# Kernel optimization log

Measured on AMD Instinct MI355X. Metric: run time of the kernel, lower is better.

## Reference

```python
import jax, jax.numpy as jnp
import numpy as np

N_NODES = 100000
N_EDGES = 3200000
N_FEAT = 256
N_HID = 64


def setup_inputs() -> dict:
    key = jax.random.key(0)
    k1, k2, k3, k4, k5 = jax.random.split(key, 5)
    edge_index = jax.random.randint(k1, (2, N_EDGES), 0, N_NODES, dtype=jnp.int64 if jax.config.jax_enable_x64 else jnp.int32)
    x = jax.random.normal(k2, (N_NODES, N_FEAT), dtype=jnp.float32)
    s_est = 1.0 / np.sqrt(N_FEAT)
    W_est = jax.random.uniform(k3, (N_FEAT, 1), jnp.float32, -s_est, s_est)
    b_est = jnp.zeros((1,), jnp.float32)
    W_gnn = jax.random.uniform(k4, (N_FEAT, N_HID), jnp.float32, -s_est, s_est)
    b_gnn = jnp.zeros((N_HID,), jnp.float32)
    s_cls = 1.0 / np.sqrt(N_HID)
    W_cls = jax.random.uniform(k5, (N_HID, 1), jnp.float32, -s_cls, s_cls)
    b_cls = jnp.zeros((1,), jnp.float32)
    return {"edge_index": edge_index, "x": x, "W_est": W_est, "b_est": b_est,
            "W_gnn": W_gnn, "b_gnn": b_gnn, "W_cls": W_cls, "b_cls": b_cls}


def _gcn_norm(edge_index, n):
    # PyG GCNConv default: add self-loops, symmetric normalization D^-1/2 (A+I) D^-1/2
    loops = jnp.arange(n, dtype=edge_index.dtype)
    row = jnp.concatenate([edge_index[0], loops])  # source
    col = jnp.concatenate([edge_index[1], loops])  # target
    deg = jax.ops.segment_sum(jnp.ones_like(col, dtype=jnp.float32), col, num_segments=n)
    dinv = jnp.where(deg > 0, jax.lax.rsqrt(jnp.maximum(deg, 1.0)), 0.0)
    norm = dinv[row] * dinv[col]  # [E+N]
    return row, col, norm


def _gcn_conv(x, W, b, row, col, norm, n):
    h = x @ W                              # [N, out] transform first (PyG order)
    msg = norm[:, None] * h[row]           # gather over sources, [E+N, out]
    out = jax.ops.segment_sum(msg, col, num_segments=n)  # scatter-add to targets
    return out + b


def reference(edge_index, x, W_est, b_est, W_gnn, b_gnn, W_cls, b_cls):
    n = x.shape[0]
    row, col, norm = _gcn_norm(edge_index, n)
    s = _gcn_conv(x, W_est, b_est, row, col, norm, n)   # estimator: GCNConv(nfeat, 1)
    z = _gcn_conv(x, W_gnn, b_gnn, row, col, norm, n)   # GNN: GCNConv(nfeat, 64)
    y = z @ W_cls + b_cls                                # classifier head
    return (y, s)
```

## Files before the change

kernel.cpp:

```cpp
#include <hip/hip_runtime.h>

#define N_NODES 100000
#define N_EDGES 3200000
#define N_FEAT  256
#define N_HID   64

#define NBINS     256
#define BIN_W     391
#define BIN_CAP   13568
#define NPART     1000
#define EPB       3200
#define I4PB      800
#define NPQ       25000
#define CPT       4

__global__ void k_wcomb(const float* __restrict__ Wg, const float* __restrict__ bg,
                        const float* __restrict__ Wc, const float* __restrict__ bc,
                        float* __restrict__ wcomb, float* __restrict__ biasy) {
    int f = threadIdx.x;
    float s = 0.f;
#pragma unroll
    for (int k = 0; k < N_HID; ++k) s += Wg[f * N_HID + k] * Wc[k];
    wcomb[f] = s;
    if (f == 0) {
        float b = 0.f;
        for (int k = 0; k < N_HID; ++k) b += bg[k] * Wc[k];
        *biasy = b + bc[0];
    }
}

__global__ __launch_bounds__(256) void k_pqhist(
        const float* __restrict__ x, const float* __restrict__ West,
        const float* __restrict__ wcomb, float2* __restrict__ pq,
        const int4* __restrict__ col4, int* __restrict__ hist) {
    __shared__ int h[NBINS];
    int tid = threadIdx.x;

    if (blockIdx.x >= NPART) {
        int node = (((int)blockIdx.x - NPART) << 2) + (tid >> 6);
        int lane = tid & 63;
        if (node >= N_NODES) return;
        float4 v  = ((const float4*)(x + (size_t)node * N_FEAT))[lane];
        float4 we = ((const float4*)West)[lane];
        float4 wc = ((const float4*)wcomb)[lane];
        float ps = v.x * we.x + v.y * we.y + v.z * we.z + v.w * we.w;
        float qs = v.x * wc.x + v.y * wc.y + v.z * wc.z + v.w * wc.w;
#pragma unroll
        for (int off = 32; off > 0; off >>= 1) {
            ps += __shfl_down(ps, off);
            qs += __shfl_down(qs, off);
        }
        if (lane == 0) pq[node] = make_float2(qs, ps);
        return;
    }

    h[tid] = 0;
    __syncthreads();
    int i0 = blockIdx.x * I4PB;
    for (int i = i0 + tid; i < i0 + I4PB; i += 256) {
        int4 c = col4[i];
        atomicAdd(&h[c.x / BIN_W], 1);
        atomicAdd(&h[c.y / BIN_W], 1);
        atomicAdd(&h[c.z / BIN_W], 1);
        atomicAdd(&h[c.w / BIN_W], 1);
    }
    __syncthreads();
    hist[blockIdx.x * NBINS + tid] = h[tid];
}

__global__ __launch_bounds__(256) void k_scan(const int* __restrict__ hist,
                                              int* __restrict__ base,
                                              int* __restrict__ cursor) {
    __shared__ int ps[256];
    int b = blockIdx.x, t = threadIdx.x;
    int v[CPT];
    int sum = 0;
    int c0 = t * CPT;
#pragma unroll
    for (int j = 0; j < CPT; ++j) {
        int blk = c0 + j;
        v[j] = (blk < NPART) ? hist[blk * NBINS + b] : 0;
        sum += v[j];
    }
    ps[t] = sum;
    __syncthreads();
#pragma unroll
    for (int d = 1; d < 256; d <<= 1) {
        int x = (t >= d) ? ps[t - d] : 0;
        __syncthreads();
        ps[t] += x;
        __syncthreads();
    }
    int run = ps[t] - sum;
#pragma unroll
    for (int j = 0; j < CPT; ++j) {
        int blk = c0 + j;
        if (blk < NPART) { base[blk * NBINS + b] = run; run += v[j]; }
    }
    if (t == 255) cursor[b] = ps[255];
}

__global__ __launch_bounds__(256) void k_scatter(const int4* __restrict__ row4,
                                                 const int4* __restrict__ col4,
                                                 const int* __restrict__ hist,
                                                 const int* __restrict__ base,
                                                 unsigned int* __restrict__ grouped) {
    __shared__ int cnts[NBINS];
    __shared__ int lstart[NBINS];
    __shared__ int lcount[NBINS];
    __shared__ int gbase[NBINS];
    __shared__ int scan[NBINS];
    __shared__ unsigned int stage[EPB];
    int tid = threadIdx.x;
    int cnt = hist[blockIdx.x * NBINS + tid];
    cnts[tid]   = cnt;
    gbase[tid]  = base[blockIdx.x * NBINS + tid];
    scan[tid]   = cnt;
    lcount[tid] = 0;
    __syncthreads();
#pragma unroll
    for (int d = 1; d < 256; d <<= 1) {
        int t = (tid >= d) ? scan[tid - d] : 0;
        __syncthreads();
        scan[tid] += t;
        __syncthreads();
    }
    lstart[tid] = scan[tid] - cnt;
    __syncthreads();

    int i0 = blockIdx.x * I4PB;
    for (int i = i0 + tid; i < i0 + I4PB; i += 256) {
        int4 c = col4[i];
        int4 r = row4[i];
        int b0 = c.x / BIN_W; int s0 = lstart[b0] + atomicAdd(&lcount[b0], 1);
        stage[s0] = ((unsigned)(c.x - b0 * BIN_W) << 17) | (unsigned)r.x;
        int b1 = c.y / BIN_W; int s1 = lstart[b1] + atomicAdd(&lcount[b1], 1);
        stage[s1] = ((unsigned)(c.y - b1 * BIN_W) << 17) | (unsigned)r.y;
        int b2 = c.z / BIN_W; int s2 = lstart[b2] + atomicAdd(&lcount[b2], 1);
        stage[s2] = ((unsigned)(c.z - b2 * BIN_W) << 17) | (unsigned)r.z;
        int b3 = c.w / BIN_W; int s3 = lstart[b3] + atomicAdd(&lcount[b3], 1);
        stage[s3] = ((unsigned)(c.w - b3 * BIN_W) << 17) | (unsigned)r.w;
    }
    __syncthreads();

    int wid = tid >> 6, lane = tid & 63;
    for (int b = wid; b < NBINS; b += 4) {
        int s = lstart[b], len = cnts[b], gb = gbase[b];
        unsigned int* dst = grouped + (size_t)b * BIN_CAP + gb;
        for (int off = lane; off < len; off += 64)
            if (gb + off < BIN_CAP) dst[off] = stage[s + off];
    }
}

__global__ __launch_bounds__(256) void k_bindeg(const int* __restrict__ cursor,
                                                const unsigned int* __restrict__ grouped,
                                                const float2* __restrict__ pq,
                                                float* __restrict__ dinv,
                                                float2* __restrict__ table) {
    __shared__ int dh[BIN_W];
    int b = blockIdx.x, tid = threadIdx.x;
    for (int i = tid; i < BIN_W; i += 256) dh[i] = 0;
    __syncthreads();
    int cnt = cursor[b];
    if (cnt > BIN_CAP) cnt = BIN_CAP;
    const unsigned int* g = grouped + (size_t)b * BIN_CAP;
    for (int i = tid; i < cnt; i += 256) atomicAdd(&dh[g[i] >> 17], 1);
    __syncthreads();
    for (int l = tid; l < BIN_W; l += 256) {
        int node = b * BIN_W + l;
        if (node < N_NODES) {
            float di = rsqrtf((float)(dh[l] + 1));
            dinv[node] = di;
            float2 v = pq[node];
            table[node] = make_float2(di * v.x, di * v.y);
        }
    }
}

__global__ __launch_bounds__(1024) void k_binacc(const int* __restrict__ cursor,
                                                 const unsigned int* __restrict__ grouped,
                                                 const float2* __restrict__ table,
                                                 const float* __restrict__ dinv,
                                                 const float* __restrict__ biasy,
                                                 const float* __restrict__ best,
                                                 float* __restrict__ out) {
    __shared__ float tx[BIN_W];
    __shared__ float ty[BIN_W];
    int b = blockIdx.x, tid = threadIdx.x;
    for (int l = tid; l < BIN_W; l += 1024) {
        int node = b * BIN_W + l;
        float2 t = (node < N_NODES) ? table[node] : make_float2(0.f, 0.f);
        tx[l] = t.x;
        ty[l] = t.y;
    }
    __syncthreads();
    int cnt = cursor[b];
    if (cnt > BIN_CAP) cnt = BIN_CAP;
    const unsigned int* g = grouped + (size_t)b * BIN_CAP;
    const uint2* g2 = (const uint2*)g;
    int n2 = cnt >> 1;
    for (int i = tid; i < n2; i += 1024) {
        uint2 v = g2[i];
        float2 ta = table[v.x & 0x1FFFFu];
        float2 tb = table[v.y & 0x1FFFFu];
        int la = v.x >> 17, lb = v.y >> 17;
        atomicAdd(&tx[la], ta.x);
        atomicAdd(&ty[la], ta.y);
        atomicAdd(&tx[lb], tb.x);
        atomicAdd(&ty[lb], tb.y);
    }
    if (tid == 0 && (cnt & 1)) {
        unsigned int v = g[cnt - 1];
        float2 t = table[v & 0x1FFFFu];
        atomicAdd(&tx[v >> 17], t.x);
        atomicAdd(&ty[v >> 17], t.y);
    }
    __syncthreads();
    float by = biasy[0], bs = best[0];
    for (int l = tid; l < BIN_W; l += 1024) {
        int node = b * BIN_W + l;
        if (node < N_NODES) {
            float di = dinv[node];
            out[node]           = di * tx[l] + by;
            out[N_NODES + node] = di * ty[l] + bs;
        }
    }
}

__global__ __launch_bounds__(256) void k_deg_fb(const int* __restrict__ col,
                                                int* __restrict__ deg) {
    int e = blockIdx.x * blockDim.x + threadIdx.x;
    if (e < N_EDGES) atomicAdd(&deg[col[e]], 1);
}
__global__ __launch_bounds__(256) void k_pqtable_fb(
        const float* __restrict__ x, const float* __restrict__ West,
        const float* __restrict__ wcomb, const int* __restrict__ deg,
        float* __restrict__ dinv, float2* __restrict__ table,
        float2* __restrict__ acc) {
    int node = (blockIdx.x * blockDim.x + threadIdx.x) >> 6;
    int lane = threadIdx.x & 63;
    if (node >= N_NODES) return;
    float4 v  = ((const float4*)(x + (size_t)node * N_FEAT))[lane];
    float4 we = ((const float4*)West)[lane];
    float4 wc = ((const float4*)wcomb)[lane];
    float ps = v.x * we.x + v.y * we.y + v.z * we.z + v.w * we.w;
    float qs = v.x * wc.x + v.y * wc.y + v.z * wc.z + v.w * wc.w;
#pragma unroll
    for (int off = 32; off > 0; off >>= 1) {
        ps += __shfl_down(ps, off);
        qs += __shfl_down(qs, off);
    }
    if (lane == 0) {
        float di = rsqrtf((float)(deg[node] + 1));
        float2 t = make_float2(di * qs, di * ps);
        dinv[node] = di; table[node] = t; acc[node] = t;
    }
}
__global__ __launch_bounds__(256) void k_edge_fb(const int* __restrict__ ei,
                                                 const float2* __restrict__ table,
                                                 float2* __restrict__ acc) {
    int e = blockIdx.x * blockDim.x + threadIdx.x;
    if (e >= N_EDGES) return;
    float2 t = table[ei[e]];
    int c = ei[N_EDGES + e];
    unsafeAtomicAdd(&acc[c].x, t.x);
    unsafeAtomicAdd(&acc[c].y, t.y);
}
__global__ __launch_bounds__(256) void k_fin_fb(
        const float* __restrict__ dinv, const float2* __restrict__ acc,
        const float* __restrict__ biasy, const float* __restrict__ best,
        float* __restrict__ out) {
    int i = blockIdx.x * blockDim.x + threadIdx.x;
    if (i >= N_NODES) return;
    float di = dinv[i];
    float2 a = acc[i];
    out[i]           = di * a.x + biasy[0];
    out[N_NODES + i] = di * a.y + best[0];
}

extern "C" void kernel_launch(void* const* d_in, const int* in_sizes, int n_in,
                              void* d_out, int out_size, void* d_ws, size_t ws_size,
                              hipStream_t stream) {
    const int*   ei   = (const int*)d_in[0];
    const float* x    = (const float*)d_in[1];
    const float* West = (const float*)d_in[2];
    const float* best = (const float*)d_in[3];
    const float* Wg   = (const float*)d_in[4];
    const float* bg   = (const float*)d_in[5];
    const float* Wc   = (const float*)d_in[6];
    const float* bc   = (const float*)d_in[7];
    float* out = (float*)d_out;

    char* ws = (char*)d_ws;
    float*  wcomb = (float*)ws;
    float*  biasy = wcomb + 256;
    float2* pq    = (float2*)(ws + 2048);
    float2* table = (float2*)(ws + 802048);
    float*  dinv  = (float*)(ws + 1602048);
    int*    cursor= (int*)(ws + 2002048);
    unsigned int* grouped = (unsigned int*)(ws + 2003072);
    int*    hist  = (int*)(ws + 2003072 + (size_t)NBINS * BIN_CAP * 4);
    int*    base  = hist + (size_t)NPART * NBINS;
    size_t need = 2003072 + (size_t)NBINS * BIN_CAP * 4 + (size_t)NPART * NBINS * 8;

    if (ws_size >= need) {
        k_wcomb<<<1, 256, 0, stream>>>(Wg, bg, Wc, bc, wcomb, biasy);
        k_pqhist<<<NPART + NPQ, 256, 0, stream>>>(x, West, wcomb, pq,
                                                  (const int4*)(ei + N_EDGES), hist);
        k_scan<<<NBINS, 256, 0, stream>>>(hist, base, cursor);
        k_scatter<<<NPART, 256, 0, stream>>>((const int4*)ei,
                                             (const int4*)(ei + N_EDGES),
                                             hist, base, grouped);
        k_bindeg<<<NBINS, 256, 0, stream>>>(cursor, grouped, pq, dinv, table);
        k_binacc<<<NBINS, 1024, 0, stream>>>(cursor, grouped, table, dinv,
                                             biasy, best, out);
    } else {
        int*    deg  = (int*)(ws + 2048 + 800000 * 2 + 400000);
        float2* acc  = pq;
        float2* tbl  = table;
        hipMemsetAsync(deg, 0, N_NODES * sizeof(int), stream);
        k_wcomb<<<1, 256, 0, stream>>>(Wg, bg, Wc, bc, wcomb, biasy);
        k_deg_fb<<<(N_EDGES + 255) / 256, 256, 0, stream>>>(ei + N_EDGES, deg);
        k_pqtable_fb<<<(N_NODES * 64 + 255) / 256, 256, 0, stream>>>(
            x, West, wcomb, deg, dinv, tbl, acc);
        k_edge_fb<<<(N_EDGES + 255) / 256, 256, 0, stream>>>(ei, tbl, acc);
        k_fin_fb<<<(N_NODES + 255) / 256, 256, 0, stream>>>(dinv, acc, biasy, best, out);
    }
}
```

Measured before the change: 107.7 us.

## Fuse weight combine into histogram kernel and move node matvec into scatter

The tiny weight-combination kernel is folded into block 0 of the histogram kernel, removing one launch. The per-node x·w projection blocks move from the histogram kernel to the scatter kernel, so the histogram and scan run shorter and the dense read of x overlaps with the edge scatter. The projection blocks now inherit the scatter kernel's larger shared-memory footprint, which may reduce occupancy for the bandwidth-bound x read.

```diff
diff --git a/kernel.cpp b/kernel.cpp
--- a/kernel.cpp
+++ b/kernel.cpp
@@ -14,26 +14,82 @@
 #define NPQ       25000
 #define CPT       4
 
-__global__ void k_wcomb(const float* __restrict__ Wg, const float* __restrict__ bg,
-                        const float* __restrict__ Wc, const float* __restrict__ bc,
-                        float* __restrict__ wcomb, float* __restrict__ biasy) {
-    int f = threadIdx.x;
-    float s = 0.f;
-#pragma unroll
-    for (int k = 0; k < N_HID; ++k) s += Wg[f * N_HID + k] * Wc[k];
-    wcomb[f] = s;
-    if (f == 0) {
-        float b = 0.f;
-        for (int k = 0; k < N_HID; ++k) b += bg[k] * Wc[k];
-        *biasy = b + bc[0];
-    }
-}
-
-__global__ __launch_bounds__(256) void k_pqhist(
+__global__ __launch_bounds__(256) void k_histw(
+        const int4* __restrict__ col4, int* __restrict__ hist,
+        const float* __restrict__ Wg, const float* __restrict__ bg,
+        const float* __restrict__ Wc, const float* __restrict__ bc,
+        float* __restrict__ wcomb, float* __restrict__ biasy) {
+    __shared__ int h[NBINS];
+    int tid = threadIdx.x;
+    if (blockIdx.x == 0) {
+        float s = 0.f;
+#pragma unroll
+        for (int k = 0; k < N_HID; ++k) s += Wg[tid * N_HID + k] * Wc[k];
+        wcomb[tid] = s;
+        if (tid == 0) {
+            float b = 0.f;
+            for (int k = 0; k < N_HID; ++k) b += bg[k] * Wc[k];
+            *biasy = b + bc[0];
+        }
+    }
+    h[tid] = 0;
+    __syncthreads();
+    int i0 = blockIdx.x * I4PB;
+    for (int i = i0 + tid; i < i0 + I4PB; i += 256) {
+        int4 c = col4[i];
+        atomicAdd(&h[c.x / BIN_W], 1);
+        atomicAdd(&h[c.y / BIN_W], 1);
+        atomicAdd(&h[c.z / BIN_W], 1);
+        atomicAdd(&h[c.w / BIN_W], 1);
+    }
+    __syncthreads();
+    hist[blockIdx.x * NBINS + tid] = h[tid];
+}
+
+__global__ __launch_bounds__(256) void k_scan(const int* __restrict__ hist,
+                                              int* __restrict__ base,
+                                              int* __restrict__ cursor) {
+    __shared__ int ps[256];
+    int b = blockIdx.x, t = threadIdx.x;
+    int v[CPT];
+    int sum = 0;
+    int c0 = t * CPT;
+#pragma unroll
+    for (int j = 0; j < CPT; ++j) {
+        int blk = c0 + j;
+        v[j] = (blk < NPART) ? hist[blk * NBINS + b] : 0;
+        sum += v[j];
+    }
+    ps[t] = sum;
+    __syncthreads();
+#pragma unroll
+    for (int d = 1; d < 256; d <<= 1) {
+        int x = (t >= d) ? ps[t - d] : 0;
+        __syncthreads();
+        ps[t] += x;
+        __syncthreads();
+    }
+    int run = ps[t] - sum;
+#pragma unroll
+    for (int j = 0; j < CPT; ++j) {
+        int blk = c0 + j;
+        if (blk < NPART) { base[blk * NBINS + b] = run; run += v[j]; }
+    }
+    if (t == 255) cursor[b] = ps[255];
+}
+
+__global__ __launch_bounds__(256) void k_scatpq(
+        const int4* __restrict__ row4, const int4* __restrict__ col4,
+        const int* __restrict__ hist, const int* __restrict__ base,
+        unsigned int* __restrict__ grouped,
         const float* __restrict__ x, const float* __restrict__ West,
-        const float* __restrict__ wcomb, float2* __restrict__ pq,
-        const int4* __restrict__ col4, int* __restrict__ hist) {
-    __shared__ int h[NBINS];
+        const float* __restrict__ wcomb, float2* __restrict__ pq) {
+    __shared__ int cnts[NBINS];
+    __shared__ int lstart[NBINS];
+    __shared__ int lcount[NBINS];
+    __shared__ int gbase[NBINS];
+    __shared__ int scan[NBINS];
+    __shared__ unsigned int stage[EPB];
     int tid = threadIdx.x;
 
     if (blockIdx.x >= NPART) {
@@ -54,64 +110,6 @@
         return;
     }
 
-    h[tid] = 0;
-    __syncthreads();
-    int i0 = blockIdx.x * I4PB;
-    for (int i = i0 + tid; i < i0 + I4PB; i += 256) {
-        int4 c = col4[i];
-        atomicAdd(&h[c.x / BIN_W], 1);
-        atomicAdd(&h[c.y / BIN_W], 1);
-        atomicAdd(&h[c.z / BIN_W], 1);
-        atomicAdd(&h[c.w / BIN_W], 1);
-    }
-    __syncthreads();
-    hist[blockIdx.x * NBINS + tid] = h[tid];
-}
-
-__global__ __launch_bounds__(256) void k_scan(const int* __restrict__ hist,
-                                              int* __restrict__ base,
-                                              int* __restrict__ cursor) {
-    __shared__ int ps[256];
-    int b = blockIdx.x, t = threadIdx.x;
-    int v[CPT];
-    int sum = 0;
-    int c0 = t * CPT;
-#pragma unroll
-    for (int j = 0; j < CPT; ++j) {
-        int blk = c0 + j;
-        v[j] = (blk < NPART) ? hist[blk * NBINS + b] : 0;
-        sum += v[j];
-    }
-    ps[t] = sum;
-    __syncthreads();
-#pragma unroll
-    for (int d = 1; d < 256; d <<= 1) {
-        int x = (t >= d) ? ps[t - d] : 0;
-        __syncthreads();
-        ps[t] += x;
-        __syncthreads();
-    }
-    int run = ps[t] - sum;
-#pragma unroll
-    for (int j = 0; j < CPT; ++j) {
-        int blk = c0 + j;
-        if (blk < NPART) { base[blk * NBINS + b] = run; run += v[j]; }
-    }
-    if (t == 255) cursor[b] = ps[255];
-}
-
-__global__ __launch_bounds__(256) void k_scatter(const int4* __restrict__ row4,
-                                                 const int4* __restrict__ col4,
-                                                 const int* __restrict__ hist,
-                                                 const int* __restrict__ base,
-                                                 unsigned int* __restrict__ grouped) {
-    __shared__ int cnts[NBINS];
-    __shared__ int lstart[NBINS];
-    __shared__ int lcount[NBINS];
-    __shared__ int gbase[NBINS];
-    __shared__ int scan[NBINS];
-    __shared__ unsigned int stage[EPB];
-    int tid = threadIdx.x;
     int cnt = hist[blockIdx.x * NBINS + tid];
     cnts[tid]   = cnt;
     gbase[tid]  = base[blockIdx.x * NBINS + tid];
@@ -227,6 +225,20 @@
     }
 }
 
+__global__ void k_wcomb_fb(const float* __restrict__ Wg, const float* __restrict__ bg,
+                           const float* __restrict__ Wc, const float* __restrict__ bc,
+                           float* __restrict__ wcomb, float* __restrict__ biasy) {
+    int f = threadIdx.x;
+    float s = 0.f;
+#pragma unroll
+    for (int k = 0; k < N_HID; ++k) s += Wg[f * N_HID + k] * Wc[k];
+    wcomb[f] = s;
+    if (f == 0) {
+        float b = 0.f;
+        for (int k = 0; k < N_HID; ++k) b += bg[k] * Wc[k];
+        *biasy = b + bc[0];
+    }
+}
 __global__ __launch_bounds__(256) void k_deg_fb(const int* __restrict__ col,
                                                 int* __restrict__ deg) {
     int e = blockIdx.x * blockDim.x + threadIdx.x;
@@ -304,13 +316,13 @@
     size_t need = 2003072 + (size_t)NBINS * BIN_CAP * 4 + (size_t)NPART * NBINS * 8;
 
     if (ws_size >= need) {
-        k_wcomb<<<1, 256, 0, stream>>>(Wg, bg, Wc, bc, wcomb, biasy);
-        k_pqhist<<<NPART + NPQ, 256, 0, stream>>>(x, West, wcomb, pq,
-                                                  (const int4*)(ei + N_EDGES), hist);
+        k_histw<<<NPART, 256, 0, stream>>>((const int4*)(ei + N_EDGES), hist,
+                                           Wg, bg, Wc, bc, wcomb, biasy);
         k_scan<<<NBINS, 256, 0, stream>>>(hist, base, cursor);
-        k_scatter<<<NPART, 256, 0, stream>>>((const int4*)ei,
-                                             (const int4*)(ei + N_EDGES),
-                                             hist, base, grouped);
+        k_scatpq<<<NPART + NPQ, 256, 0, stream>>>((const int4*)ei,
+                                                  (const int4*)(ei + N_EDGES),
+                                                  hist, base, grouped,
+                                                  x, West, wcomb, pq);
         k_bindeg<<<NBINS, 256, 0, stream>>>(cursor, grouped, pq, dinv, table);
         k_binacc<<<NBINS, 1024, 0, stream>>>(cursor, grouped, table, dinv,
                                              biasy, best, out);
@@ -319,7 +331,7 @@
         float2* acc  = pq;
         float2* tbl  = table;
         hipMemsetAsync(deg, 0, N_NODES * sizeof(int), stream);
-        k_wcomb<<<1, 256, 0, stream>>>(Wg, bg, Wc, bc, wcomb, biasy);
+        k_wcomb_fb<<<1, 256, 0, stream>>>(Wg, bg, Wc, bc, wcomb, biasy);
         k_deg_fb<<<(N_EDGES + 255) / 256, 256, 0, stream>>>(ei + N_EDGES, deg);
         k_pqtable_fb<<<(N_NODES * 64 + 255) / 256, 256, 0, stream>>>(
             x, West, wcomb, deg, dinv, tbl, acc);
```

Measured after the change: 97.17 us. 9.8% less time.
